# Kernel tuning notes

Measured on AMD Instinct MI355X. Metric: run time of the kernel, lower is better.

## Reference

```python
import jax, jax.numpy as jnp
import numpy as np

J = 24          # SMPL_NR_JOINTS
H = 24          # hidden_dim
D_IN = 3        # input_dim (xyz)
SMPL_PARENTS = [-1, 0, 0, 0, 1, 2, 3, 4, 5, 6, 7, 8, 9, 9, 9, 12, 13, 14, 16, 17, 18, 19, 20, 21]

def _build_A():
    # undirected kinematic tree + self loops, row-normalized (mean aggregation)
    M = np.zeros((J, J), np.float32)
    for child, parent in enumerate(SMPL_PARENTS):
        if parent >= 0:
            M[child, parent] = 1.0
            M[parent, child] = 1.0
    M += np.eye(J, dtype=np.float32)
    M /= M.sum(axis=1, keepdims=True)
    return jnp.asarray(M)

A_NORM = _build_A()  # [J, J]

def setup_inputs() -> dict:
    key = jax.random.key(0)
    ks = jax.random.split(key, 12)
    B, S, T = 2048, 24, 24
    g = lambda k, shape, s=0.1: jax.random.normal(k, shape, dtype=jnp.float32) * s
    return {
        "src": g(ks[0], (B, S, J, D_IN), 1.0),
        "tgt": g(ks[1], (B, T, J, D_IN), 1.0),
        "We": g(ks[2], (H, D_IN)), "be": jnp.zeros((H,), jnp.float32),
        # gate order: 0=i, 1=f, 2=c, 3=o
        "Wxl": g(ks[3], (4, H, H)), "bxl": jnp.zeros((4, H), jnp.float32),
        "Wxr": g(ks[4], (4, H, H)),
        "Whl": g(ks[5], (4, H, H)), "bhl": jnp.zeros((4, H), jnp.float32),
        "Whr": g(ks[6], (4, H, H)),
        "wg": g(ks[7], (3, H)),   # peephole weights for i, f, o
        "bg": jnp.zeros((4, H), jnp.float32),
        "Wd": g(ks[8], (D_IN * J, H * J)), "bd": jnp.zeros((D_IN * J,), jnp.float32),
    }

def _gconv(x, Wl, bl, Wr):
    # x: [B, J, D]; mean-aggregate over fixed 24-node graph, then l(agg) + r(x)
    agg = jnp.einsum('ij,bjd->bid', A_NORM, x)
    return agg @ Wl.T + bl + x @ Wr.T

def _cell(X, h, c, Wxl, bxl, Wxr, Whl, bhl, Whr, wg, bg):
    gx = lambda g: _gconv(X, Wxl[g], bxl[g], Wxr[g])
    gh = lambda g: _gconv(h, Whl[g], bhl[g], Whr[g])
    i = jax.nn.sigmoid(gx(0) + gh(0) + wg[0] * c + bg[0])
    f = jax.nn.sigmoid(gx(1) + gh(1) + wg[1] * c + bg[1])
    c_new = f * c + i * jnp.tanh(gx(2) + gh(2) + bg[2])
    o = jax.nn.sigmoid(gx(3) + gh(3) + wg[2] * c_new + bg[3])
    h_new = o * jnp.tanh(c_new)
    return o, h_new, c_new

def reference(src, tgt, We, be, Wxl, bxl, Wxr, Whl, bhl, Whr, wg, bg, Wd, bd):
    B, S = src.shape[0], src.shape[1]
    T = tgt.shape[1]
    params = (Wxl, bxl, Wxr, Whl, bhl, Whr, wg, bg)
    enc = lambda x: jax.nn.relu(x @ We.T + be)  # [B, J, H]

    # --- warm-up over last 24 src frames (deterministic: encode only first step) ---
    X0 = enc(src[:, S - 24])
    h = jnp.zeros((B, J, H), src.dtype)
    c = jnp.zeros((B, J, H), src.dtype)
    out, h, c = _cell(X0, h, c, *params)

    def warm_step(carry, _):
        o_, h_, c_ = carry
        o_, h_, c_ = _cell(o_, h_, c_, *params)
        return (o_, h_, c_), None
    (out, h, c), _ = jax.lax.scan(warm_step, (out, h, c), None, length=23)

    # --- decode T steps: first input is enc(tgt[:,0]), then feed previous out ---
    out0, h, c = _cell(enc(tgt[:, 0]), h, c, *params)

    def dec_step(carry, _):
        o_, h_, c_ = carry
        o2, h2, c2 = _cell(o_, h_, c_, *params)
        return (o2, h2, c2), o2
    _, rest = jax.lax.scan(dec_step, (out0, h, c), None, length=T - 1)  # [T-1, B, J, H]

    seq = jnp.concatenate([out0[None], rest], axis=0)            # [T, B, J, H]
    outs = seq.transpose(1, 0, 2, 3).reshape(B, T, J * H)        # [B, T, 576]
    return outs @ Wd.T + bd                                      # [B, T, 72]
```

## Files before the change

### kernel.cpp

```cpp
#include <hip/hip_runtime.h>


typedef short s16x8 __attribute__((ext_vector_type(8)));
typedef float f32x4 __attribute__((ext_vector_type(4)));

#define TPB 192
#define NB 2
#define PQ_OFF 0
#define UO_OFF 19968
#define SMEM_SZ 26880

__device__ __forceinline__ unsigned short f2b(float f) {
    unsigned int x = __float_as_uint(f);
    x = x + 0x7fffu + ((x >> 16) & 1u);
    return (unsigned short)(x >> 16);
}
__device__ __forceinline__ unsigned int pk2(float a, float b) {
    return (unsigned int)f2b(a) | ((unsigned int)f2b(b) << 16);
}
__device__ __forceinline__ float frcp(float x) { return __builtin_amdgcn_rcpf(x); }
__device__ __forceinline__ float sigm(float x) {
    float t = __expf(-x);
    return frcp(1.0f + t);
}
__device__ __forceinline__ float tanh_(float x) {
    float xc = fmaxf(x, -30.f);
    float t = __expf(-2.f * xc);
    return (1.f - t) * frcp(1.f + t);
}

extern "C" __global__ void __launch_bounds__(TPB, 3)
gclstm_main(const float* __restrict__ src,
            const float* __restrict__ tgt,
            const float* __restrict__ We,
            const float* __restrict__ be,
            const float* __restrict__ Wxl,
            const float* __restrict__ bxl,
            const float* __restrict__ Wxr,
            const float* __restrict__ Whl,
            const float* __restrict__ bhl,
            const float* __restrict__ Whr,
            const float* __restrict__ wg,
            const float* __restrict__ bg,
            unsigned short* __restrict__ seqh)
{
    __shared__ __align__(16) char smem[SMEM_SZ];
    unsigned short* PQt = (unsigned short*)(smem + PQ_OFF);
    unsigned short* UO  = (unsigned short*)(smem + UO_OFF);

    const int tid = threadIdx.x;
    const int b0 = blockIdx.x * NB;
    const int lane = tid & 63, wid = tid >> 6;
    const int l15 = lane & 15, quad = lane >> 4;

    const int par[24] = {-1,0,0,0,1,2,3,4,5,6,7,8,9,9,9,12,13,14,16,17,18,19,20,21};

    s16x8 w1f[4][2];
#pragma unroll
    for (int cj = 0; cj < 4; ++cj) {
        int np = (wid * 4 + cj) * 16 + l15;
        int path = np >= 96 ? 1 : 0;
        int nn = np - path * 96;
        int g = nn / 24, d = nn - g * 24;
        const float* Wx = path ? Wxr : Wxl;
        const float* Wh = path ? Whr : Whl;
#pragma unroll
        for (int kt = 0; kt < 2; ++kt) {
            s16x8 f;
#pragma unroll
            for (int kk = 0; kk < 8; ++kk) {
                int k = kt * 32 + quad * 8 + kk;
                float v = 0.f;
                if (k < 24) v = Wx[g * 576 + d * 24 + k];
                else if (k < 48) v = Wh[g * 576 + d * 24 + (k - 24)];
                f[kk] = (short)f2b(v);
            }
            w1f[cj][kt] = f;
        }
    }

    s16x8 mf[3];
    {
        int i = wid * 16 + l15;
        int si = i / 24, ji = i - si * 24;
        int cnt = 1 + (par[ji] >= 0 ? 1 : 0);
#pragma unroll
        for (int ch = 0; ch < 24; ++ch) cnt += (par[ch] == ji) ? 1 : 0;
        float cntf = (float)cnt;
#pragma unroll
        for (int kt = 0; kt < 3; ++kt) {
            s16x8 f;
#pragma unroll
            for (int kk = 0; kk < 8; ++kk) {
                int jp = kt * 32 + quad * 8 + kk;
                float v = 0.f;
                if (jp < 48) {
                    int sj = jp / 24, jj = jp - sj * 24;
                    if (sj == si && (jj == ji || par[jj] == ji || par[ji] == jj)) v = 1.f;
                } else {
                    if (jp - 48 == i) v = cntf;
                }
                f[kk] = (short)f2b(v);
            }
            mf[kt] = f;
        }
    }

    const int d1 = l15;
    const int d2 = 16 + (l15 & 7);
    float bC1[4], bC2[4], wv1[3], wv2[3];
#pragma unroll
    for (int g = 0; g < 4; ++g) {
        bC1[g] = bxl[g * 24 + d1] + bhl[g * 24 + d1] + bg[g * 24 + d1];
        bC2[g] = bxl[g * 24 + d2] + bhl[g * 24 + d2] + bg[g * 24 + d2];
    }
#pragma unroll
    for (int p = 0; p < 3; ++p) { wv1[p] = wg[p * 24 + d1]; wv2[p] = wg[p * 24 + d2]; }

    int rowR[4];
    float iwR[4];
    long long sb[4];
#pragma unroll
    for (int rr = 0; rr < 4; ++rr) {
        int row = wid * 16 + quad * 4 + rr;
        rowR[rr] = row;
        int j = row % 24;
        int cnt = 1 + (par[j] >= 0 ? 1 : 0);
#pragma unroll
        for (int ch = 0; ch < 24; ++ch) cnt += (par[ch] == j) ? 1 : 0;
        iwR[rr] = cnt == 2 ? 0.5f : cnt == 3 ? (1.f / 3.f) : cnt == 4 ? 0.25f : 0.2f;
        sb[rr] = (long long)(b0 + row / 24) * 13824 + (long long)j * 24;
    }

    float c1[4] = {0.f, 0.f, 0.f, 0.f};
    float c2[2] = {0.f, 0.f};

#pragma unroll
    for (int t = 0; t < 3; ++t) {
        int task = tid + t * TPB;
        int row = task / 12, dp = task - row * 12;
        int b = b0 + row / 24, j = row % 24;
        const float* sp = src + (size_t)b * 1728 + j * 3;
        float s0 = sp[0], s1 = sp[1], s2 = sp[2];
        int d = 2 * dp;
        float x0 = be[d] + s0 * We[d * 3] + s1 * We[d * 3 + 1] + s2 * We[d * 3 + 2];
        float x1 = be[d + 1] + s0 * We[d * 3 + 3] + s1 * We[d * 3 + 4] + s2 * We[d * 3 + 5];
        x0 = fmaxf(x0, 0.f); x1 = fmaxf(x1, 0.f);
        *(unsigned int*)(UO + row * 72 + d) = pk2(x0, x1);
        *(unsigned int*)(UO + row * 72 + 24 + d) = 0u;
        *(unsigned int*)(UO + row * 72 + 48 + d) = 0u;
    }
    __syncthreads();

    for (int s = 0; s < 48; ++s) {
        if (s == 24) {
#pragma unroll
            for (int t = 0; t < 3; ++t) {
                int task = tid + t * TPB;
                int row = task / 12, dp = task - row * 12;
                int b = b0 + row / 24, j = row % 24;
                const float* tp = tgt + (size_t)b * 1728 + j * 3;
                float s0 = tp[0], s1 = tp[1], s2 = tp[2];
                int d = 2 * dp;
                float x0 = be[d] + s0 * We[d * 3] + s1 * We[d * 3 + 1] + s2 * We[d * 3 + 2];
                float x1 = be[d + 1] + s0 * We[d * 3 + 3] + s1 * We[d * 3 + 4]
                         + s2 * We[d * 3 + 5];
                x0 = fmaxf(x0, 0.f); x1 = fmaxf(x1, 0.f);
                *(unsigned int*)(UO + row * 72 + d) = pk2(x0, x1);
            }
            __syncthreads();
        }

        f32x4 acc1[3][4];
#pragma unroll
        for (int rt = 0; rt < 3; ++rt)
#pragma unroll
            for (int cj = 0; cj < 4; ++cj) acc1[rt][cj] = (f32x4)0.f;
#pragma unroll
        for (int kt = 0; kt < 2; ++kt) {
            s16x8 a[3];
#pragma unroll
            for (int rt = 0; rt < 3; ++rt)
                a[rt] = *(const s16x8*)(UO + (rt * 16 + l15) * 72 + kt * 32 + quad * 8);
#pragma unroll
            for (int rt = 0; rt < 3; ++rt)
#pragma unroll
                for (int cj = 0; cj < 4; ++cj)
                    acc1[rt][cj] = __builtin_amdgcn_mfma_f32_16x16x32_bf16(a[rt], w1f[cj][kt], acc1[rt][cj], 0, 0, 0);
        }
#pragma unroll
        for (int rt = 0; rt < 3; ++rt)
#pragma unroll
            for (int cj = 0; cj < 4; ++cj) {
                int np = (wid * 4 + cj) * 16 + l15;
                int r96 = np >= 96 ? np - 96 : np;
                int col = (np >= 96 ? 48 : 0) + rt * 16 + quad * 4;
                uint2 wv;
                wv.x = pk2(acc1[rt][cj][0], acc1[rt][cj][1]);
                wv.y = pk2(acc1[rt][cj][2], acc1[rt][cj][3]);
                *(uint2*)(PQt + r96 * 104 + col) = wv;
            }
        __syncthreads();

        f32x4 acc2[6];
#pragma unroll
        for (int nt = 0; nt < 6; ++nt) acc2[nt] = (f32x4)0.f;
#pragma unroll
        for (int kt = 0; kt < 3; ++kt) {
            if (kt == 2 && wid == 0) continue;
            s16x8 bf[6];
#pragma unroll
            for (int nt = 0; nt < 6; ++nt)
                bf[nt] = *(const s16x8*)(PQt + (nt * 16 + l15) * 104 + kt * 32 + quad * 8);
#pragma unroll
            for (int nt = 0; nt < 6; ++nt)
                acc2[nt] = __builtin_amdgcn_mfma_f32_16x16x32_bf16(mf[kt], bf[nt], acc2[nt], 0, 0, 0);
        }

        const bool lo = l15 < 8;
#pragma unroll
        for (int rr = 0; rr < 4; ++rr) {
            float a0 = acc2[0][rr], a1 = acc2[1][rr], a2 = acc2[2][rr];
            float a3 = acc2[3][rr], a4 = acc2[4][rr], a5 = acc2[5][rr];
            float x1 = __shfl_xor(a1, 8);
            float x2 = __shfl_xor(a2, 8);
            float x4 = __shfl_xor(a4, 8);
            float x5 = __shfl_xor(a5, 8);
            float iw = iwR[rr];
            int row = rowR[rr];
            {
                float c = c1[rr];
                float pi = fmaf(iw, a0, bC1[0]);
                float pf = fmaf(iw, lo ? x1 : x2, bC1[1]);
                float pc = fmaf(iw, a3, bC1[2]);
                float po = fmaf(iw, lo ? x4 : x5, bC1[3]);
                float iv = sigm(fmaf(wv1[0], c, pi));
                float fv = sigm(fmaf(wv1[1], c, pf));
                float cn = fmaf(fv, c, iv * tanh_(pc));
                float ov = sigm(fmaf(wv1[2], cn, po));
                c1[rr] = cn;
                float hv = ov * tanh_(cn);
                UO[row * 72 + d1] = f2b(ov);
                UO[row * 72 + 24 + d1] = f2b(hv);
                if (s >= 24) seqh[sb[rr] + (long long)(s - 24) * 576 + d1] = f2b(ov);
            }
            {
                const bool schemeA = (rr < 2);
                bool act = schemeA ? lo : !lo;
                float g0 = schemeA ? a1 : x1;
                float g1 = schemeA ? x2 : a2;
                float g2 = schemeA ? a4 : x4;
                float g3 = schemeA ? x5 : a5;
                float c = c2[rr & 1];
                float pi = fmaf(iw, g0, bC2[0]);
                float pf = fmaf(iw, g1, bC2[1]);
                float pc = fmaf(iw, g2, bC2[2]);
                float po = fmaf(iw, g3, bC2[3]);
                float iv = sigm(fmaf(wv2[0], c, pi));
                float fv = sigm(fmaf(wv2[1], c, pf));
                float cn = fmaf(fv, c, iv * tanh_(pc));
                float ov = sigm(fmaf(wv2[2], cn, po));
                float hv = ov * tanh_(cn);
                if (act) {
                    c2[rr & 1] = cn;
                    UO[row * 72 + d2] = f2b(ov);
                    UO[row * 72 + 24 + d2] = f2b(hv);
                    if (s >= 24) seqh[sb[rr] + (long long)(s - 24) * 576 + d2] = f2b(ov);
                }
            }
        }
        __syncthreads();
    }
}

extern "C" __global__ void __launch_bounds__(256)
wd_conv(const float* __restrict__ Wd, unsigned short* __restrict__ WdH)
{
    int i = blockIdx.x * 256 + threadIdx.x;
    if (i < 46080) {
        int n = i / 576, k = i - n * 576;
        WdH[i] = (n < 72) ? f2b(Wd[n * 576 + k]) : (unsigned short)0;
    }
}

template <int PRECONV>
__global__ void __launch_bounds__(256, 4)
gclstm_proj(const unsigned short* __restrict__ seqh,
            const unsigned short* __restrict__ WdH,
            const float* __restrict__ Wd,
            const float* __restrict__ bd,
            float* __restrict__ out)
{
    __shared__ unsigned short SQ[64 * 104];
    __shared__ unsigned short WH[80 * 104];

    const int tid = threadIdx.x;
    const int R0 = blockIdx.x * 64;
    const int lane = tid & 63, wid = tid >> 6;
    const int l15 = lane & 15, quad = lane >> 4;

    f32x4 acc[5];
#pragma unroll
    for (int j = 0; j < 5; ++j) acc[j] = (f32x4)0.f;

    if (PRECONV) {
        s16x8 sreg[3], wreg[4];
#pragma unroll
        for (int j = 0; j < 3; ++j) {
            int i = tid + j * 256; int r = i / 12, c8 = i - r * 12;
            sreg[j] = *(const s16x8*)(seqh + (size_t)(R0 + r) * 576 + (size_t)(c8 * 8));
        }
#pragma unroll
        for (int j = 0; j < 4; ++j) {
            int i = tid + j * 256;
            if (i < 960) { int n = i / 12, c8 = i - n * 12;
                wreg[j] = *(const s16x8*)(WdH + (size_t)n * 576 + (size_t)(c8 * 8)); }
        }
        for (int kc = 0; kc < 576; kc += 96) {
#pragma unroll
            for (int j = 0; j < 3; ++j) {
                int i = tid + j * 256; int r = i / 12, c8 = i - r * 12;
                *(s16x8*)(&SQ[r * 104 + c8 * 8]) = sreg[j];
            }
#pragma unroll
            for (int j = 0; j < 4; ++j) {
                int i = tid + j * 256;
                if (i < 960) { int n = i / 12, c8 = i - n * 12;
                    *(s16x8*)(&WH[n * 104 + c8 * 8]) = wreg[j]; }
            }
            __syncthreads();
            if (kc + 96 < 576) {
#pragma unroll
                for (int j = 0; j < 3; ++j) {
                    int i = tid + j * 256; int r = i / 12, c8 = i - r * 12;
                    sreg[j] = *(const s16x8*)(seqh + (size_t)(R0 + r) * 576 + (size_t)(kc + 96 + c8 * 8));
                }
#pragma unroll
                for (int j = 0; j < 4; ++j) {
                    int i = tid + j * 256;
                    if (i < 960) { int n = i / 12, c8 = i - n * 12;
                        wreg[j] = *(const s16x8*)(WdH + (size_t)n * 576 + (size_t)(kc + 96 + c8 * 8)); }
                }
            }
#pragma unroll
            for (int kt = 0; kt < 3; ++kt) {
                int koff = kt * 32 + quad * 8;
                s16x8 a = *(const s16x8*)(&SQ[(wid * 16 + l15) * 104 + koff]);
#pragma unroll
                for (int j = 0; j < 5; ++j) {
                    s16x8 b = *(const s16x8*)(&WH[(j * 16 + l15) * 104 + koff]);
                    acc[j] = __builtin_amdgcn_mfma_f32_16x16x32_bf16(a, b, acc[j], 0, 0, 0);
                }
            }
            __syncthreads();
        }
    } else {
        for (int kc = 0; kc < 576; kc += 96) {
            __syncthreads();
            for (int i = tid; i < 768; i += 256) {
                int r = i / 12, c8 = i - r * 12;
                *(s16x8*)(&SQ[r * 104 + c8 * 8]) =
                    *(const s16x8*)(seqh + (size_t)(R0 + r) * 576 + (size_t)(kc + c8 * 8));
            }
            for (int i = tid; i < 7680; i += 256) {
                int n = i / 96, kk = i - n * 96;
                float v = (n < 72) ? Wd[(size_t)n * 576 + (size_t)(kc + kk)] : 0.f;
                WH[n * 104 + kk] = f2b(v);
            }
            __syncthreads();
#pragma unroll
            for (int kt = 0; kt < 3; ++kt) {
                int koff = kt * 32 + quad * 8;
                s16x8 a = *(const s16x8*)(&SQ[(wid * 16 + l15) * 104 + koff]);
#pragma unroll
                for (int j = 0; j < 5; ++j) {
                    s16x8 b = *(const s16x8*)(&WH[(j * 16 + l15) * 104 + koff]);
                    acc[j] = __builtin_amdgcn_mfma_f32_16x16x32_bf16(a, b, acc[j], 0, 0, 0);
                }
            }
        }
    }

#pragma unroll
    for (int j = 0; j < 5; ++j) {
        int n = j * 16 + l15;
        if (n < 72) {
            float bv = bd[n];
            int rbase = R0 + wid * 16 + quad * 4;
#pragma unroll
            for (int r = 0; r < 4; ++r)
                out[(size_t)(rbase + r) * 72 + (size_t)n] = acc[j][r] + bv;
        }
    }
}

extern "C" void kernel_launch(void* const* d_in, const int* in_sizes, int n_in,
                              void* d_out, int out_size, void* d_ws, size_t ws_size,
                              hipStream_t stream)
{
    const float* src = (const float*)d_in[0];
    const float* tgt = (const float*)d_in[1];
    const float* We  = (const float*)d_in[2];
    const float* be  = (const float*)d_in[3];
    const float* Wxl = (const float*)d_in[4];
    const float* bxl = (const float*)d_in[5];
    const float* Wxr = (const float*)d_in[6];
    const float* Whl = (const float*)d_in[7];
    const float* bhl = (const float*)d_in[8];
    const float* Whr = (const float*)d_in[9];
    const float* wg  = (const float*)d_in[10];
    const float* bg  = (const float*)d_in[11];
    const float* Wd  = (const float*)d_in[12];
    const float* bd  = (const float*)d_in[13];
    float* out = (float*)d_out;
    unsigned short* seqh = (unsigned short*)d_ws;

    const size_t seq_bytes = (size_t)2048 * 24 * 576 * 2;
    unsigned short* WdH = (unsigned short*)((char*)d_ws + seq_bytes);
    const bool preconv = ws_size >= seq_bytes + (size_t)80 * 576 * 2;

    if (preconv)
        wd_conv<<<dim3(180), dim3(256), 0, stream>>>(Wd, WdH);
    gclstm_main<<<dim3(1024), dim3(TPB), 0, stream>>>(
        src, tgt, We, be, Wxl, bxl, Wxr, Whl, bhl, Whr, wg, bg, seqh);
    if (preconv)
        gclstm_proj<1><<<dim3(768), dim3(256), 0, stream>>>(seqh, WdH, Wd, bd, out);
    else
        gclstm_proj<0><<<dim3(768), dim3(256), 0, stream>>>(seqh, nullptr, Wd, bd, out);
}
```

Baseline: 376.9 us.

## Rework PQ layout to skip zero MFMA tile, lighter barriers, smaller proj tiles

In the recurrent kernel, the PQ staging layout and aggregation matrix are reordered so wave 2 can skip one all-zero k-tile of the second MFMA. The second-half gate evaluation now computes only the two active rows instead of four with predication. __syncthreads is replaced by an LDS-only waitcnt plus s_barrier. The projection kernel switches to 32-row blocks with twice as many blocks and a higher launch-bounds occupancy target, which adds more redundant loads of Wd per block.

```diff
diff --git a/kernel.cpp b/kernel.cpp
--- a/kernel.cpp
+++ b/kernel.cpp
@@ -9,6 +9,9 @@
 #define PQ_OFF 0
 #define UO_OFF 19968
 #define SMEM_SZ 26880
+
+#define BAR() do { asm volatile("s_waitcnt lgkmcnt(0)" ::: "memory"); \
+                   __builtin_amdgcn_s_barrier(); } while (0)
 
 __device__ __forceinline__ unsigned short f2b(float f) {
     unsigned int x = __float_as_uint(f);
@@ -93,12 +96,14 @@
 #pragma unroll
             for (int kk = 0; kk < 8; ++kk) {
                 int jp = kt * 32 + quad * 8 + kk;
+                int sj = jp / 48;
+                int rem = jp - sj * 48;
+                int pz = rem / 24;
+                int j = rem - pz * 24;
                 float v = 0.f;
-                if (jp < 48) {
-                    int sj = jp / 24, jj = jp - sj * 24;
-                    if (sj == si && (jj == ji || par[jj] == ji || par[ji] == jj)) v = 1.f;
-                } else {
-                    if (jp - 48 == i) v = cntf;
+                if (sj == si) {
+                    if (pz == 0) v = (j == ji || par[j] == ji || par[ji] == j) ? 1.f : 0.f;
+                    else         v = (j == ji) ? cntf : 0.f;
                 }
                 f[kk] = (short)f2b(v);
             }
@@ -108,6 +113,7 @@
 
     const int d1 = l15;
     const int d2 = 16 + (l15 & 7);
+    const bool lo = l15 < 8;
     float bC1[4], bC2[4], wv1[3], wv2[3];
 #pragma unroll
     for (int g = 0; g < 4; ++g) {
@@ -130,6 +136,12 @@
         for (int ch = 0; ch < 24; ++ch) cnt += (par[ch] == j) ? 1 : 0;
         iwR[rr] = cnt == 2 ? 0.5f : cnt == 3 ? (1.f / 3.f) : cnt == 4 ? 0.25f : 0.2f;
         sb[rr] = (long long)(b0 + row / 24) * 13824 + (long long)j * 24;
+    }
+    int row2v[2]; float iw2v[2]; long long sb2v[2];
+#pragma unroll
+    for (int e = 0; e < 2; ++e) {
+        int rsel = lo ? e : e + 2;
+        row2v[e] = rowR[rsel]; iw2v[e] = iwR[rsel]; sb2v[e] = sb[rsel];
     }
 
     float c1[4] = {0.f, 0.f, 0.f, 0.f};
@@ -168,7 +180,7 @@
                 x0 = fmaxf(x0, 0.f); x1 = fmaxf(x1, 0.f);
                 *(unsigned int*)(UO + row * 72 + d) = pk2(x0, x1);
             }
-            __syncthreads();
+            BAR();
         }
 
         f32x4 acc1[3][4];
@@ -193,14 +205,16 @@
 #pragma unroll
             for (int cj = 0; cj < 4; ++cj) {
                 int np = (wid * 4 + cj) * 16 + l15;
-                int r96 = np >= 96 ? np - 96 : np;
-                int col = (np >= 96 ? 48 : 0) + rt * 16 + quad * 4;
+                int path = np >= 96;
+                int nn = np - (path ? 96 : 0);
+                int jg = rt * 16 + quad * 4;
+                int col = (path ? 24 : 0) + jg + (jg >= 24 ? 24 : 0);
                 uint2 wv;
                 wv.x = pk2(acc1[rt][cj][0], acc1[rt][cj][1]);
                 wv.y = pk2(acc1[rt][cj][2], acc1[rt][cj][3]);
-                *(uint2*)(PQt + r96 * 104 + col) = wv;
-            }
-        __syncthreads();
+                *(uint2*)(PQt + nn * 104 + col) = wv;
+            }
+        BAR();
 
         f32x4 acc2[6];
 #pragma unroll
@@ -208,6 +222,7 @@
 #pragma unroll
         for (int kt = 0; kt < 3; ++kt) {
             if (kt == 2 && wid == 0) continue;
+            if (kt == 0 && wid == 2) continue;
             s16x8 bf[6];
 #pragma unroll
             for (int nt = 0; nt < 6; ++nt)
@@ -217,59 +232,55 @@
                 acc2[nt] = __builtin_amdgcn_mfma_f32_16x16x32_bf16(mf[kt], bf[nt], acc2[nt], 0, 0, 0);
         }
 
-        const bool lo = l15 < 8;
+        const long long so = (long long)(s - 24) * 576;
+
 #pragma unroll
         for (int rr = 0; rr < 4; ++rr) {
-            float a0 = acc2[0][rr], a1 = acc2[1][rr], a2 = acc2[2][rr];
-            float a3 = acc2[3][rr], a4 = acc2[4][rr], a5 = acc2[5][rr];
-            float x1 = __shfl_xor(a1, 8);
-            float x2 = __shfl_xor(a2, 8);
-            float x4 = __shfl_xor(a4, 8);
-            float x5 = __shfl_xor(a5, 8);
+            float pf_s = __shfl_xor(lo ? acc2[2][rr] : acc2[1][rr], 8);
+            float po_s = __shfl_xor(lo ? acc2[5][rr] : acc2[4][rr], 8);
             float iw = iwR[rr];
             int row = rowR[rr];
-            {
-                float c = c1[rr];
-                float pi = fmaf(iw, a0, bC1[0]);
-                float pf = fmaf(iw, lo ? x1 : x2, bC1[1]);
-                float pc = fmaf(iw, a3, bC1[2]);
-                float po = fmaf(iw, lo ? x4 : x5, bC1[3]);
-                float iv = sigm(fmaf(wv1[0], c, pi));
-                float fv = sigm(fmaf(wv1[1], c, pf));
-                float cn = fmaf(fv, c, iv * tanh_(pc));
-                float ov = sigm(fmaf(wv1[2], cn, po));
-                c1[rr] = cn;
-                float hv = ov * tanh_(cn);
-                UO[row * 72 + d1] = f2b(ov);
-                UO[row * 72 + 24 + d1] = f2b(hv);
-                if (s >= 24) seqh[sb[rr] + (long long)(s - 24) * 576 + d1] = f2b(ov);
-            }
-            {
-                const bool schemeA = (rr < 2);
-                bool act = schemeA ? lo : !lo;
-                float g0 = schemeA ? a1 : x1;
-                float g1 = schemeA ? x2 : a2;
-                float g2 = schemeA ? a4 : x4;
-                float g3 = schemeA ? x5 : a5;
-                float c = c2[rr & 1];
-                float pi = fmaf(iw, g0, bC2[0]);
-                float pf = fmaf(iw, g1, bC2[1]);
-                float pc = fmaf(iw, g2, bC2[2]);
-                float po = fmaf(iw, g3, bC2[3]);
-                float iv = sigm(fmaf(wv2[0], c, pi));
-                float fv = sigm(fmaf(wv2[1], c, pf));
-                float cn = fmaf(fv, c, iv * tanh_(pc));
-                float ov = sigm(fmaf(wv2[2], cn, po));
-                float hv = ov * tanh_(cn);
-                if (act) {
-                    c2[rr & 1] = cn;
-                    UO[row * 72 + d2] = f2b(ov);
-                    UO[row * 72 + 24 + d2] = f2b(hv);
-                    if (s >= 24) seqh[sb[rr] + (long long)(s - 24) * 576 + d2] = f2b(ov);
-                }
-            }
-        }
-        __syncthreads();
+            float c = c1[rr];
+            float pi = fmaf(iw, acc2[0][rr], bC1[0]);
+            float pf = fmaf(iw, pf_s, bC1[1]);
+            float pc = fmaf(iw, acc2[3][rr], bC1[2]);
+            float po = fmaf(iw, po_s, bC1[3]);
+            float iv = sigm(fmaf(wv1[0], c, pi));
+            float fv = sigm(fmaf(wv1[1], c, pf));
+            float cn = fmaf(fv, c, iv * tanh_(pc));
+            float ov = sigm(fmaf(wv1[2], cn, po));
+            c1[rr] = cn;
+            float hv = ov * tanh_(cn);
+            UO[row * 72 + d1] = f2b(ov);
+            UO[row * 72 + 24 + d1] = f2b(hv);
+            if (s >= 24) seqh[sb[rr] + so + d1] = f2b(ov);
+        }
+#pragma unroll
+        for (int e = 0; e < 2; ++e) {
+            float sA = __shfl_xor(lo ? acc2[1][e + 2] : acc2[2][e], 8);
+            float sB = __shfl_xor(lo ? acc2[4][e + 2] : acc2[5][e], 8);
+            float g0 = lo ? acc2[1][e] : sA;
+            float g1 = lo ? sA : acc2[2][e + 2];
+            float g2 = lo ? acc2[4][e] : sB;
+            float g3 = lo ? sB : acc2[5][e + 2];
+            float iw = iw2v[e];
+            int row = row2v[e];
+            float c = c2[e];
+            float pi = fmaf(iw, g0, bC2[0]);
+            float pf = fmaf(iw, g1, bC2[1]);
+            float pc = fmaf(iw, g2, bC2[2]);
+            float po = fmaf(iw, g3, bC2[3]);
+            float iv = sigm(fmaf(wv2[0], c, pi));
+            float fv = sigm(fmaf(wv2[1], c, pf));
+            float cn = fmaf(fv, c, iv * tanh_(pc));
+            float ov = sigm(fmaf(wv2[2], cn, po));
+            c2[e] = cn;
+            float hv = ov * tanh_(cn);
+            UO[row * 72 + d2] = f2b(ov);
+            UO[row * 72 + 24 + d2] = f2b(hv);
+            if (s >= 24) seqh[sb2v[e] + so + d2] = f2b(ov);
+        }
+        BAR();
     }
 }
 
@@ -284,32 +295,36 @@
 }
 
 template <int PRECONV>
-__global__ void __launch_bounds__(256, 4)
+__global__ void __launch_bounds__(256, 6)
 gclstm_proj(const unsigned short* __restrict__ seqh,
             const unsigned short* __restrict__ WdH,
             const float* __restrict__ Wd,
             const float* __restrict__ bd,
             float* __restrict__ out)
 {
-    __shared__ unsigned short SQ[64 * 104];
+    __shared__ unsigned short SQ[32 * 104];
     __shared__ unsigned short WH[80 * 104];
 
     const int tid = threadIdx.x;
-    const int R0 = blockIdx.x * 64;
+    const int R0 = blockIdx.x * 32;
     const int lane = tid & 63, wid = tid >> 6;
     const int l15 = lane & 15, quad = lane >> 4;
-
-    f32x4 acc[5];
-#pragma unroll
-    for (int j = 0; j < 5; ++j) acc[j] = (f32x4)0.f;
+    const int rt = wid & 1;
+    const int c0 = (wid < 2) ? 0 : 3;
+    const int nct = (wid < 2) ? 3 : 2;
+
+    f32x4 acc[3];
+#pragma unroll
+    for (int j = 0; j < 3; ++j) acc[j] = (f32x4)0.f;
 
     if (PRECONV) {
-        s16x8 sreg[3], wreg[4];
-#pragma unroll
-        for (int j = 0; j < 3; ++j) {
-            int i = tid + j * 256; int r = i / 12, c8 = i - r * 12;
-            sreg[j] = *(const s16x8*)(seqh + (size_t)(R0 + r) * 576 + (size_t)(c8 * 8));
-        }
+        s16x8 sreg[2], wreg[4];
+        const int r0s = tid / 12, c0s = tid - r0s * 12;
+        const int i1 = tid + 256;
+        const int r1s = i1 / 12, c1s = i1 - r1s * 12;
+        sreg[0] = *(const s16x8*)(seqh + (size_t)(R0 + r0s) * 576 + (size_t)(c0s * 8));
+        if (tid < 128)
+            sreg[1] = *(const s16x8*)(seqh + (size_t)(R0 + r1s) * 576 + (size_t)(c1s * 8));
 #pragma unroll
         for (int j = 0; j < 4; ++j) {
             int i = tid + j * 256;
@@ -317,24 +332,19 @@
                 wreg[j] = *(const s16x8*)(WdH + (size_t)n * 576 + (size_t)(c8 * 8)); }
         }
         for (int kc = 0; kc < 576; kc += 96) {
-#pragma unroll
-            for (int j = 0; j < 3; ++j) {
-                int i = tid + j * 256; int r = i / 12, c8 = i - r * 12;
-                *(s16x8*)(&SQ[r * 104 + c8 * 8]) = sreg[j];
-            }
+            *(s16x8*)(&SQ[r0s * 104 + c0s * 8]) = sreg[0];
+            if (tid < 128) *(s16x8*)(&SQ[r1s * 104 + c1s * 8]) = sreg[1];
 #pragma unroll
             for (int j = 0; j < 4; ++j) {
                 int i = tid + j * 256;
                 if (i < 960) { int n = i / 12, c8 = i - n * 12;
                     *(s16x8*)(&WH[n * 104 + c8 * 8]) = wreg[j]; }
             }
-            __syncthreads();
+            BAR();
             if (kc + 96 < 576) {
-#pragma unroll
-                for (int j = 0; j < 3; ++j) {
-                    int i = tid + j * 256; int r = i / 12, c8 = i - r * 12;
-                    sreg[j] = *(const s16x8*)(seqh + (size_t)(R0 + r) * 576 + (size_t)(kc + 96 + c8 * 8));
-                }
+                sreg[0] = *(const s16x8*)(seqh + (size_t)(R0 + r0s) * 576 + (size_t)(kc + 96 + c0s * 8));
+                if (tid < 128)
+                    sreg[1] = *(const s16x8*)(seqh + (size_t)(R0 + r1s) * 576 + (size_t)(kc + 96 + c1s * 8));
 #pragma unroll
                 for (int j = 0; j < 4; ++j) {
                     int i = tid + j * 256;
@@ -345,19 +355,21 @@
 #pragma unroll
             for (int kt = 0; kt < 3; ++kt) {
                 int koff = kt * 32 + quad * 8;
-                s16x8 a = *(const s16x8*)(&SQ[(wid * 16 + l15) * 104 + koff]);
-#pragma unroll
-                for (int j = 0; j < 5; ++j) {
-                    s16x8 b = *(const s16x8*)(&WH[(j * 16 + l15) * 104 + koff]);
-                    acc[j] = __builtin_amdgcn_mfma_f32_16x16x32_bf16(a, b, acc[j], 0, 0, 0);
+                s16x8 a = *(const s16x8*)(&SQ[(rt * 16 + l15) * 104 + koff]);
+#pragma unroll
+                for (int j = 0; j < 3; ++j) {
+                    if (j < nct) {
+                        s16x8 b = *(const s16x8*)(&WH[((c0 + j) * 16 + l15) * 104 + koff]);
+                        acc[j] = __builtin_amdgcn_mfma_f32_16x16x32_bf16(a, b, acc[j], 0, 0, 0);
+                    }
                 }
             }
-            __syncthreads();
+            BAR();
         }
     } else {
         for (int kc = 0; kc < 576; kc += 96) {
             __syncthreads();
-            for (int i = tid; i < 768; i += 256) {
+            for (int i = tid; i < 384; i += 256) {
                 int r = i / 12, c8 = i - r * 12;
                 *(s16x8*)(&SQ[r * 104 + c8 * 8]) =
                     *(const s16x8*)(seqh + (size_t)(R0 + r) * 576 + (size_t)(kc + c8 * 8));
@@ -371,25 +383,29 @@
 #pragma unroll
             for (int kt = 0; kt < 3; ++kt) {
                 int koff = kt * 32 + quad * 8;
-                s16x8 a = *(const s16x8*)(&SQ[(wid * 16 + l15) * 104 + koff]);
-#pragma unroll
-                for (int j = 0; j < 5; ++j) {
-                    s16x8 b = *(const s16x8*)(&WH[(j * 16 + l15) * 104 + koff]);
-                    acc[j] = __builtin_amdgcn_mfma_f32_16x16x32_bf16(a, b, acc[j], 0, 0, 0);
+                s16x8 a = *(const s16x8*)(&SQ[(rt * 16 + l15) * 104 + koff]);
+#pragma unroll
+                for (int j = 0; j < 3; ++j) {
+                    if (j < nct) {
+                        s16x8 b = *(const s16x8*)(&WH[((c0 + j) * 16 + l15) * 104 + koff]);
+                        acc[j] = __builtin_amdgcn_mfma_f32_16x16x32_bf16(a, b, acc[j], 0, 0, 0);
+                    }
                 }
             }
         }
     }
 
 #pragma unroll
-    for (int j = 0; j < 5; ++j) {
-        int n = j * 16 + l15;
-        if (n < 72) {
-            float bv = bd[n];
-            int rbase = R0 + wid * 16 + quad * 4;
-#pragma unroll
-            for (int r = 0; r < 4; ++r)
-                out[(size_t)(rbase + r) * 72 + (size_t)n] = acc[j][r] + bv;
+    for (int j = 0; j < 3; ++j) {
+        if (j < nct) {
+            int n = (c0 + j) * 16 + l15;
+            if (n < 72) {
+                float bv = bd[n];
+                int rbase = R0 + rt * 16 + quad * 4;
+#pragma unroll
+                for (int r = 0; r < 4; ++r)
+                    out[(size_t)(rbase + r) * 72 + (size_t)n] = acc[j][r] + bv;
+            }
         }
     }
 }
@@ -424,7 +440,7 @@
     gclstm_main<<<dim3(1024), dim3(TPB), 0, stream>>>(
         src, tgt, We, be, Wxl, bxl, Wxr, Whl, bhl, Whr, wg, bg, seqh);
     if (preconv)
-        gclstm_proj<1><<<dim3(768), dim3(256), 0, stream>>>(seqh, WdH, Wd, bd, out);
+        gclstm_proj<1><<<dim3(1536), dim3(256), 0, stream>>>(seqh, WdH, Wd, bd, out);
     else
-        gclstm_proj<0><<<dim3(768), dim3(256), 0, stream>>>(seqh, nullptr, Wd, bd, out);
-}
+        gclstm_proj<0><<<dim3(1536), dim3(256), 0, stream>>>(seqh, nullptr, Wd, bd, out);
+}
```

After: 357.0 us. 5.3% less time.
